# Optimization experiments

Hardware: AMD Instinct MI355X
Metric: run time of the kernel (lower is better)

## Reference

```python
import jax, jax.numpy as jnp
import numpy as np

N = 100_000      # nodes
E = 1_600_000    # edges (avg degree 16)
C_IN, C_H, C_OUT = 32, 64, 64
G = 64           # graphs in batch


def setup_inputs() -> dict:
    key = jax.random.key(0)
    ks = jax.random.split(key, 10)
    x = jax.random.normal(ks[0], (N, C_IN), jnp.float32)
    edge_index = jax.random.randint(ks[1], (2, E), 0, N, dtype=jnp.int64)
    edge_weight = jax.random.uniform(ks[2], (E,), jnp.float32)
    batch = jnp.sort(jax.random.randint(ks[3], (N,), 0, G, dtype=jnp.int64))
    def lin(k, fan_in, fan_out):
        return jax.random.normal(k, (fan_in, fan_out), jnp.float32) / np.float32(np.sqrt(fan_in))
    W1 = lin(ks[4], C_IN, C_H)
    W2 = lin(ks[5], C_H, C_H)
    W3 = lin(ks[6], C_H, C_OUT)
    b1 = jnp.zeros((C_H,), jnp.float32)
    b2 = jnp.zeros((C_H,), jnp.float32)
    b3 = jnp.zeros((C_OUT,), jnp.float32)
    return {"x": x, "edge_weight": edge_weight, "W1": W1, "b1": b1,
            "W2": W2, "b2": b2, "W3": W3, "b3": b3,
            "edge_index": edge_index, "batch": batch}


def _gcn_norm(edge_index, edge_weight, n):
    # PyG GCNConv default: add self-loops (weight 1), symmetric D^-1/2 A D^-1/2 norm.
    loop = jnp.arange(n, dtype=edge_index.dtype)
    src = jnp.concatenate([edge_index[0], loop])
    dst = jnp.concatenate([edge_index[1], loop])
    ew = jnp.concatenate([edge_weight, jnp.ones((n,), edge_weight.dtype)])
    deg = jax.ops.segment_sum(ew, dst, num_segments=n)
    dis = jnp.where(deg > 0, jax.lax.rsqrt(deg), jnp.float32(0))
    norm = dis[src] * ew * dis[dst]
    return src, dst, norm


def _gcn_layer(h, W, b, src, dst, norm, n):
    h = h @ W                                 # [N, out]
    msg = h[src] * norm[:, None]              # gather + scale  [E+N, out]
    agg = jax.ops.segment_sum(msg, dst, num_segments=n)
    return agg + b


def reference(x, edge_weight, W1, b1, W2, b2, W3, b3, edge_index, batch):
    n = x.shape[0]
    src, dst, norm = _gcn_norm(edge_index, edge_weight, n)  # shared across layers
    h = jax.nn.silu(_gcn_layer(x, W1, b1, src, dst, norm, n))
    # Dropout(0.1) is identity in eval mode
    h = jax.nn.silu(_gcn_layer(h, W2, b2, src, dst, norm, n))
    h = jax.nn.silu(_gcn_layer(h, W3, b3, src, dst, norm, n))
    # global_mean_pool over graphs
    sums = jax.ops.segment_sum(h, batch, num_segments=G)
    counts = jax.ops.segment_sum(jnp.ones((n,), h.dtype), batch, num_segments=G)
    return sums / jnp.maximum(counts, 1)[:, None]
```

## Files before the change

kernel.cpp:

```cpp
#include <hip/hip_runtime.h>
#include <hip/hip_fp16.h>
#include <math.h>


#define NB   256
#define PBLK 1024
#define FIXP_SCALE 1048576.0f
#define FIXP_MASK  ((1ULL << 40) - 1)

__device__ __forceinline__ int lower_bound_i(const int* __restrict__ a, int n, int v) {
    int lo = 0, hi = n;
    while (lo < hi) {
        int m = (lo + hi) >> 1;
        if (a[m] < v) lo = m + 1; else hi = m;
    }
    return lo;
}

__global__ __launch_bounds__(256) void k_bhist(const int* __restrict__ dst,
                                               int* __restrict__ hcnt, int e) {
    __shared__ int hist[NB];
    int tid = threadIdx.x, blk = blockIdx.x;
    hist[tid] = 0;
    __syncthreads();
    int chunk = (e + PBLK - 1) / PBLK;
    int lo = blk * chunk, hi = min(e, lo + chunk);
    for (int i = lo + tid; i < hi; i += 256)
        atomicAdd(&hist[dst[i] >> 9], 1);
    __syncthreads();
    hcnt[tid * PBLK + blk] = hist[tid];
}

__global__ __launch_bounds__(256) void k_bscan(int* __restrict__ hcnt,
                                               int* __restrict__ btot) {
    __shared__ int s[256];
    int b = blockIdx.x, tid = threadIdx.x;
    int* row = hcnt + b * PBLK;
    int a0 = row[4 * tid], a1 = row[4 * tid + 1], a2 = row[4 * tid + 2], a3 = row[4 * tid + 3];
    int tsum = a0 + a1 + a2 + a3;
    s[tid] = tsum;
    __syncthreads();
    for (int off = 1; off < 256; off <<= 1) {
        int t = (tid >= off) ? s[tid - off] : 0;
        __syncthreads();
        s[tid] += t;
        __syncthreads();
    }
    int ex = s[tid] - tsum;
    row[4 * tid] = ex;
    row[4 * tid + 1] = ex + a0;
    row[4 * tid + 2] = ex + a0 + a1;
    row[4 * tid + 3] = ex + a0 + a1 + a2;
    if (tid == 255) btot[b] = s[255];
}

__global__ __launch_bounds__(256) void k_bbase(const int* __restrict__ btot,
                                               int* __restrict__ bbase,
                                               int* __restrict__ rowptr, int n, int e) {
    __shared__ int s[256];
    int tid = threadIdx.x;
    int v = btot[tid];
    s[tid] = v;
    __syncthreads();
    for (int off = 1; off < 256; off <<= 1) {
        int t = (tid >= off) ? s[tid - off] : 0;
        __syncthreads();
        s[tid] += t;
        __syncthreads();
    }
    bbase[tid] = s[tid] - v;
    if (tid == 255) bbase[NB] = s[255];
    if (tid == 0) rowptr[n] = e;
}

__global__ __launch_bounds__(256) void k_bpart(const int* __restrict__ src,
                                               const int* __restrict__ dst,
                                               const float* __restrict__ ew,
                                               const int* __restrict__ hcnt,
                                               const int* __restrict__ bbase,
                                               int2* __restrict__ bedge, int e) {
    __shared__ int cur[NB];
    int tid = threadIdx.x, blk = blockIdx.x;
    cur[tid] = bbase[tid] + hcnt[tid * PBLK + blk];
    __syncthreads();
    int chunk = (e + PBLK - 1) / PBLK;
    int lo = blk * chunk, hi = min(e, lo + chunk);
    for (int i = lo + tid; i < hi; i += 256) {
        int d = dst[i];
        int pos = atomicAdd(&cur[d >> 9], 1);
        bedge[pos] = make_int2(src[i] | ((d & 511) << 17), __float_as_int(ew[i]));
    }
}

__global__ __launch_bounds__(256) void k_bucket(const int2* __restrict__ bedge,
                                                const int* __restrict__ bbase,
                                                float* __restrict__ dis,
                                                int* __restrict__ rowptr,
                                                int2* __restrict__ em, int n) {
    __shared__ unsigned long long pk[512];
    __shared__ int cnt[512];
    __shared__ int scn[512];
    __shared__ float sdis[512];
    __shared__ int cur[512];
    int b = blockIdx.x, tid = threadIdx.x;
    int e0 = bbase[b], e1 = bbase[b + 1];
    pk[tid] = 0ULL; pk[tid + 256] = 0ULL;
    __syncthreads();
    for (int i = e0 + tid; i < e1; i += 256) {
        int2 v = bedge[i];
        int dlo = (v.x >> 17) & 511;
        unsigned long long p =
            (1ULL << 40) | (unsigned long long)(__int_as_float(v.y) * FIXP_SCALE);
        atomicAdd(&pk[dlo], p);
    }
    __syncthreads();
#pragma unroll
    for (int k = 0; k < 2; ++k) {
        int i = tid + k * 256;
        unsigned long long v = pk[i];
        int c = (int)(v >> 40);
        cnt[i] = c; scn[i] = c;
        sdis[i] = rsqrtf(1.0f + (float)(v & FIXP_MASK) * (1.0f / FIXP_SCALE));
    }
    __syncthreads();
    for (int off = 1; off < 512; off <<= 1) {
        int i0 = tid, i1 = tid + 256;
        int v0 = (i0 >= off) ? scn[i0 - off] : 0;
        int v1 = (i1 >= off) ? scn[i1 - off] : 0;
        __syncthreads();
        scn[i0] += v0; scn[i1] += v1;
        __syncthreads();
    }
#pragma unroll
    for (int k = 0; k < 2; ++k) {
        int i = tid + k * 256;
        int rb = e0 + scn[i] - cnt[i];
        cur[i] = rb;
        int node = (b << 9) + i;
        if (node < n) { rowptr[node] = rb; dis[node] = sdis[i]; }
    }
    __syncthreads();
    for (int i = e0 + tid; i < e1; i += 256) {
        int2 v = bedge[i];
        int dlo = (v.x >> 17) & 511;
        int pos = atomicAdd(&cur[dlo], 1);
        float w = __int_as_float(v.y) * sdis[dlo];
        em[pos] = make_int2(v.x & 0x1FFFF, __float_as_int(w));
    }
}

__global__ void k_scale(const float* __restrict__ x, const float* __restrict__ dis,
                        __half* __restrict__ hs, int total) {
    int idx = blockIdx.x * blockDim.x + threadIdx.x;
    if (idx < total) hs[idx] = __float2half(x[idx] * dis[idx >> 5]);
}

__device__ __forceinline__ float2 cvt_pair(unsigned int u) {
    __half2 h2 = *(__half2*)&u;
    return __half22float2(h2);
}

template <bool SCALE, typename OUT>
__global__ __launch_bounds__(256, 3) void k_aggmm64(const __half* __restrict__ h,
                                                    const int2* __restrict__ em,
                                                    const int* __restrict__ rowptr,
                                                    const float* __restrict__ dis,
                                                    const float* __restrict__ W,
                                                    const float* __restrict__ bias,
                                                    OUT* __restrict__ out, int n) {
    __shared__ __align__(16) float sacc[4][64];
    __shared__ __align__(8) int2 sme[4][64];
    int lane = threadIdx.x & 63, wv = threadIdx.x >> 6;
    int c = lane & 31, half = lane >> 5;
    const unsigned int* h32 = (const unsigned int*)h;
    float w[64];
#pragma unroll
    for (int k = 0; k < 64; ++k) w[k] = W[k * 64 + lane];
    float bv = bias[lane];
    int wid = (blockIdx.x * blockDim.x + threadIdx.x) >> 6;
    int nw = (gridDim.x * blockDim.x) >> 6;
    for (int node = wid; node < n; node += nw) {
#pragma unroll
        for (int k = 0; k < 64; ++k) asm volatile("" : "+v"(w[k]));
        int lo = rowptr[node], hi = rowptr[node + 1];
        int deg = hi - lo;
        float2 acc = make_float2(0.0f, 0.0f);
        if (half == 0) {
            float2 hv0 = cvt_pair(h32[(unsigned)(node * 32 + c)]);
            float di = dis[node];
            acc.x = di * hv0.x; acc.y = di * hv0.y;
        }
        for (int jb = 0; jb < deg; jb += 64) {
            int idx = lo + jb + lane;
            int2 me = (idx < hi) ? em[idx] : make_int2(0, 0);
            sme[wv][lane] = me;
            int rem = deg - jb;
#pragma unroll
            for (int g = 0; g < 4; ++g) {
                if (g * 16 < rem) {
                    int2 ev[8];
#pragma unroll
                    for (int t = 0; t < 8; ++t)
                        ev[t] = sme[wv][g * 16 + 2 * t + half];
                    unsigned int hv[8];
#pragma unroll
                    for (int t = 0; t < 8; ++t)
                        hv[t] = h32[(unsigned)(ev[t].x * 32 + c)];
#pragma unroll
                    for (int t = 0; t < 8; ++t) {
                        float ww = __int_as_float(ev[t].y);
                        float2 hf = cvt_pair(hv[t]);
                        acc.x = fmaf(ww, hf.x, acc.x);
                        acc.y = fmaf(ww, hf.y, acc.y);
                    }
                }
            }
        }
        acc.x += __shfl_down(acc.x, 32, 64);
        acc.y += __shfl_down(acc.y, 32, 64);
        if (half == 0) ((float2*)sacc[wv])[c] = acc;
        float o = bv;
        const float4* s4 = (const float4*)sacc[wv];
#pragma unroll
        for (int k4 = 0; k4 < 16; ++k4) {
            float4 a4 = s4[k4];
            o = fmaf(a4.x, w[4 * k4 + 0], o);
            o = fmaf(a4.y, w[4 * k4 + 1], o);
            o = fmaf(a4.z, w[4 * k4 + 2], o);
            o = fmaf(a4.w, w[4 * k4 + 3], o);
        }
        o = o / (1.0f + __expf(-o));
        if (SCALE) o *= dis[node];
        if (sizeof(OUT) == 2) {
            ((__half*)out)[(size_t)node * 64 + lane] = __float2half(o);
        } else {
            ((float*)out)[(size_t)node * 64 + lane] = o;
        }
    }
}

__global__ __launch_bounds__(256, 3) void k_aggmm32(const __half* __restrict__ h,
                                                    const int2* __restrict__ em,
                                                    const int* __restrict__ rowptr,
                                                    const float* __restrict__ dis,
                                                    const float* __restrict__ W,
                                                    const float* __restrict__ bias,
                                                    __half* __restrict__ out, int n) {
    __shared__ __align__(16) float sacc[4][32];
    __shared__ __align__(8) int2 sme[4][64];
    int lane = threadIdx.x & 63, wv = threadIdx.x >> 6;
    int c = lane & 15, quarter = lane >> 4;
    const unsigned int* h32 = (const unsigned int*)h;
    float w[32];
#pragma unroll
    for (int k = 0; k < 32; ++k) w[k] = W[k * 64 + lane];
    float bv = bias[lane];
    int wid = (blockIdx.x * blockDim.x + threadIdx.x) >> 6;
    int nw = (gridDim.x * blockDim.x) >> 6;
    for (int node = wid; node < n; node += nw) {
#pragma unroll
        for (int k = 0; k < 32; ++k) asm volatile("" : "+v"(w[k]));
        int lo = rowptr[node], hi = rowptr[node + 1];
        int deg = hi - lo;
        float2 acc = make_float2(0.0f, 0.0f);
        if (quarter == 0) {
            float2 hv0 = cvt_pair(h32[(unsigned)(node * 16 + c)]);
            float di = dis[node];
            acc.x = di * hv0.x; acc.y = di * hv0.y;
        }
        for (int jb = 0; jb < deg; jb += 64) {
            int idx = lo + jb + lane;
            int2 me = (idx < hi) ? em[idx] : make_int2(0, 0);
            sme[wv][lane] = me;
            int rem = deg - jb;
#pragma unroll
            for (int g = 0; g < 4; ++g) {
                if (g * 16 < rem) {
                    int2 ev[4];
#pragma unroll
                    for (int t = 0; t < 4; ++t)
                        ev[t] = sme[wv][g * 16 + 4 * t + quarter];
                    unsigned int hv[4];
#pragma unroll
                    for (int t = 0; t < 4; ++t)
                        hv[t] = h32[(unsigned)(ev[t].x * 16 + c)];
#pragma unroll
                    for (int t = 0; t < 4; ++t) {
                        float ww = __int_as_float(ev[t].y);
                        float2 hf = cvt_pair(hv[t]);
                        acc.x = fmaf(ww, hf.x, acc.x);
                        acc.y = fmaf(ww, hf.y, acc.y);
                    }
                }
            }
        }
        acc.x += __shfl_down(acc.x, 32, 64);
        acc.y += __shfl_down(acc.y, 32, 64);
        acc.x += __shfl_down(acc.x, 16, 64);
        acc.y += __shfl_down(acc.y, 16, 64);
        if (quarter == 0) ((float2*)sacc[wv])[c] = acc;
        float o = bv;
        const float4* s4 = (const float4*)sacc[wv];
#pragma unroll
        for (int k4 = 0; k4 < 8; ++k4) {
            float4 a4 = s4[k4];
            o = fmaf(a4.x, w[4 * k4 + 0], o);
            o = fmaf(a4.y, w[4 * k4 + 1], o);
            o = fmaf(a4.z, w[4 * k4 + 2], o);
            o = fmaf(a4.w, w[4 * k4 + 3], o);
        }
        o = o / (1.0f + __expf(-o));
        o *= dis[node];
        out[(size_t)node * 64 + lane] = __float2half(o);
    }
}

__global__ void k_pool_partial(const float* __restrict__ h, const int* __restrict__ batch,
                               float* __restrict__ acc, int n) {
    int c = threadIdx.x & 63, r = threadIdx.x >> 6;
    int base = blockIdx.x * 128;
    int end = base + 128; if (end > n) end = n;
    float part = 0.0f;
    int cur = -1;
    for (int i = base + r; i < end; i += 4) {
        int g = batch[i];
        if (g != cur) {
            if (cur >= 0) atomicAdd(&acc[cur * 64 + c], part);
            part = 0.0f;
            cur = g;
        }
        part += h[(size_t)i * 64 + c];
    }
    if (cur >= 0) atomicAdd(&acc[cur * 64 + c], part);
}

__global__ void k_pool_final(const float* __restrict__ acc, const int* __restrict__ batch,
                             float* __restrict__ out, int n) {
    int idx = blockIdx.x * blockDim.x + threadIdx.x;
    int g = idx >> 6;
    int lo = lower_bound_i(batch, n, g);
    int hi = lower_bound_i(batch, n, g + 1);
    int cnt = hi - lo;
    out[idx] = acc[idx] / (float)(cnt > 0 ? cnt : 1);
}

extern "C" void kernel_launch(void* const* d_in, const int* in_sizes, int n_in,
                              void* d_out, int out_size, void* d_ws, size_t ws_size,
                              hipStream_t stream) {
    const float* x   = (const float*)d_in[0];
    const float* ew  = (const float*)d_in[1];
    const float* W1  = (const float*)d_in[2];
    const float* b1  = (const float*)d_in[3];
    const float* W2  = (const float*)d_in[4];
    const float* b2  = (const float*)d_in[5];
    const float* W3  = (const float*)d_in[6];
    const float* b3  = (const float*)d_in[7];
    const int*   eidx  = (const int*)d_in[8];
    const int*   batch = (const int*)d_in[9];
    float* out = (float*)d_out;

    const int E = in_sizes[1];
    const int N = in_sizes[9];
    const int G = 64;
    const int* src = eidx;
    const int* dst = eidx + E;

    char* p = (char*)d_ws;
    __half* A     = (__half*)p;                p += (size_t)N * 64 * sizeof(__half);
    __half* B     = (__half*)p;                p += (size_t)N * 64 * sizeof(__half);
    float* C      = (float*)p;                 p += (size_t)N * 64 * sizeof(float);
    float* dis    = (float*)p;                 p += (size_t)N * sizeof(float);
    int*   rowptr = (int*)p;                   p += (size_t)(N + 1) * sizeof(int);
    int*   bbase  = (int*)p;                   p += (size_t)(NB + 1) * sizeof(int);
    float* acc    = (float*)p;                 p += (size_t)G * 64 * sizeof(float);
    p = (char*)(((uintptr_t)p + 7) & ~(uintptr_t)7);
    int2*  em     = (int2*)p;

    int2* bedge = (int2*)A;
    int*  hcnt  = (int*)B;
    int*  btot  = (int*)B + NB * PBLK;

    const int BT = 256;
    const int FUSED_BLOCKS = 3125;

    k_bhist<<<PBLK, 256, 0, stream>>>(dst, hcnt, E);
    k_bscan<<<NB, 256, 0, stream>>>(hcnt, btot);
    k_bbase<<<1, 256, 0, stream>>>(btot, bbase, rowptr, N, E);
    k_bpart<<<PBLK, 256, 0, stream>>>(src, dst, ew, hcnt, bbase, bedge, E);
    k_bucket<<<NB, 256, 0, stream>>>(bedge, bbase, dis, rowptr, em, N);

    k_scale<<<(N * 32 + BT - 1) / BT, BT, 0, stream>>>(x, dis, (__half*)B, N * 32);
    k_aggmm32<<<FUSED_BLOCKS, BT, 0, stream>>>((__half*)B, em, rowptr, dis, W1, b1, A, N);

    k_aggmm64<true, __half><<<FUSED_BLOCKS, BT, 0, stream>>>(A, em, rowptr, dis, W2, b2, B, N);

    k_aggmm64<false, float><<<FUSED_BLOCKS, BT, 0, stream>>>(B, em, rowptr, dis, W3, b3, C, N);

    hipMemsetAsync(acc, 0, (size_t)G * 64 * sizeof(float), stream);
    k_pool_partial<<<(N + 127) / 128, BT, 0, stream>>>(C, batch, acc, N);
    k_pool_final<<<(G * 64) / BT, BT, 0, stream>>>(acc, batch, out, N);
}
```

Measured before the change: 361.8 us.

## Split fused aggregate-then-matmul into separate node matmul and aggregation kernels

For layers 2 and 3, the dense 64x64 transform now runs first as a standalone per-node kernel with W held in shared memory, producing half-precision Z = Y·W. A lighter aggregation kernel then gathers Z over edges and applies bias, SiLU and the optional degree scale. This removes the 64-register weight array and the per-node shared-memory reduction from the gather kernel, so it can run at higher occupancy. The cost is an extra kernel launch per layer and an extra read and write of the node feature matrix. It also changes rounding, because the matmul result is rounded to fp16 before aggregation.

```diff
diff --git a/kernel.cpp b/kernel.cpp
--- a/kernel.cpp
+++ b/kernel.cpp
@@ -160,35 +160,68 @@
     return __half22float2(h2);
 }
 
+__global__ __launch_bounds__(256, 2) void k_mm64(const __half* __restrict__ y,
+                                                 const float* __restrict__ W,
+                                                 __half* __restrict__ z, int n) {
+    __shared__ float sw[64 * 64];
+#pragma unroll
+    for (int i = 0; i < 16; ++i)
+        sw[threadIdx.x + 256 * i] = W[threadIdx.x + 256 * i];
+    __syncthreads();
+    int node = blockIdx.x * 256 + threadIdx.x;
+    if (node >= n) return;
+    uint4 yp[8];
+    const uint4* yrow = (const uint4*)(y + (size_t)node * 64);
+#pragma unroll
+    for (int i = 0; i < 8; ++i) yp[i] = yrow[i];
+    const unsigned int* ypk = (const unsigned int*)yp;
+    float o[64];
+#pragma unroll
+    for (int j = 0; j < 64; ++j) o[j] = 0.0f;
+#pragma unroll
+    for (int k2 = 0; k2 < 32; ++k2) {
+        float2 yk = cvt_pair(ypk[k2]);
+        const float4* r0 = (const float4*)&sw[(2 * k2) * 64];
+        const float4* r1 = (const float4*)&sw[(2 * k2 + 1) * 64];
+#pragma unroll
+        for (int j4 = 0; j4 < 16; ++j4) {
+            float4 w0 = r0[j4];
+            float4 w1 = r1[j4];
+            o[4 * j4 + 0] = fmaf(yk.y, w1.x, fmaf(yk.x, w0.x, o[4 * j4 + 0]));
+            o[4 * j4 + 1] = fmaf(yk.y, w1.y, fmaf(yk.x, w0.y, o[4 * j4 + 1]));
+            o[4 * j4 + 2] = fmaf(yk.y, w1.z, fmaf(yk.x, w0.z, o[4 * j4 + 2]));
+            o[4 * j4 + 3] = fmaf(yk.y, w1.w, fmaf(yk.x, w0.w, o[4 * j4 + 3]));
+        }
+    }
+    __half2* zrow = (__half2*)(z + (size_t)node * 64);
+#pragma unroll
+    for (int j2 = 0; j2 < 32; ++j2)
+        zrow[j2] = __float22half2_rn(make_float2(o[2 * j2], o[2 * j2 + 1]));
+}
+
 template <bool SCALE, typename OUT>
-__global__ __launch_bounds__(256, 3) void k_aggmm64(const __half* __restrict__ h,
-                                                    const int2* __restrict__ em,
-                                                    const int* __restrict__ rowptr,
-                                                    const float* __restrict__ dis,
-                                                    const float* __restrict__ W,
-                                                    const float* __restrict__ bias,
-                                                    OUT* __restrict__ out, int n) {
-    __shared__ __align__(16) float sacc[4][64];
+__global__ __launch_bounds__(256, 4) void k_agg64(const __half* __restrict__ z,
+                                                  const int2* __restrict__ em,
+                                                  const int* __restrict__ rowptr,
+                                                  const float* __restrict__ dis,
+                                                  const float* __restrict__ bias,
+                                                  OUT* __restrict__ out, int n) {
     __shared__ __align__(8) int2 sme[4][64];
     int lane = threadIdx.x & 63, wv = threadIdx.x >> 6;
     int c = lane & 31, half = lane >> 5;
-    const unsigned int* h32 = (const unsigned int*)h;
-    float w[64];
-#pragma unroll
-    for (int k = 0; k < 64; ++k) w[k] = W[k * 64 + lane];
-    float bv = bias[lane];
+    const unsigned int* h32 = (const unsigned int*)z;
+    float2 bv2 = ((const float2*)bias)[c];
     int wid = (blockIdx.x * blockDim.x + threadIdx.x) >> 6;
     int nw = (gridDim.x * blockDim.x) >> 6;
     for (int node = wid; node < n; node += nw) {
-#pragma unroll
-        for (int k = 0; k < 64; ++k) asm volatile("" : "+v"(w[k]));
         int lo = rowptr[node], hi = rowptr[node + 1];
         int deg = hi - lo;
+        float di = 0.0f;
         float2 acc = make_float2(0.0f, 0.0f);
         if (half == 0) {
-            float2 hv0 = cvt_pair(h32[(unsigned)(node * 32 + c)]);
-            float di = dis[node];
-            acc.x = di * hv0.x; acc.y = di * hv0.y;
+            di = dis[node];
+            float2 hv = cvt_pair(h32[(unsigned)(node * 32 + c)]);
+            acc.x = di * hv.x; acc.y = di * hv.y;
         }
         for (int jb = 0; jb < deg; jb += 64) {
             int idx = lo + jb + lane;
@@ -218,23 +251,17 @@
         }
         acc.x += __shfl_down(acc.x, 32, 64);
         acc.y += __shfl_down(acc.y, 32, 64);
-        if (half == 0) ((float2*)sacc[wv])[c] = acc;
-        float o = bv;
-        const float4* s4 = (const float4*)sacc[wv];
-#pragma unroll
-        for (int k4 = 0; k4 < 16; ++k4) {
-            float4 a4 = s4[k4];
-            o = fmaf(a4.x, w[4 * k4 + 0], o);
-            o = fmaf(a4.y, w[4 * k4 + 1], o);
-            o = fmaf(a4.z, w[4 * k4 + 2], o);
-            o = fmaf(a4.w, w[4 * k4 + 3], o);
-        }
-        o = o / (1.0f + __expf(-o));
-        if (SCALE) o *= dis[node];
-        if (sizeof(OUT) == 2) {
-            ((__half*)out)[(size_t)node * 64 + lane] = __float2half(o);
-        } else {
-            ((float*)out)[(size_t)node * 64 + lane] = o;
+        if (half == 0) {
+            float ox = acc.x + bv2.x, oy = acc.y + bv2.y;
+            ox = ox / (1.0f + __expf(-ox));
+            oy = oy / (1.0f + __expf(-oy));
+            if (SCALE) { ox *= di; oy *= di; }
+            if (sizeof(OUT) == 2) {
+                ((__half2*)out)[(size_t)node * 32 + c] =
+                    __float22half2_rn(make_float2(ox, oy));
+            } else {
+                ((float2*)out)[(size_t)node * 32 + c] = make_float2(ox, oy);
+            }
         }
     }
 }
@@ -382,6 +409,7 @@
 
     const int BT = 256;
     const int FUSED_BLOCKS = 3125;
+    const int MM_BLOCKS = (N + 255) / 256;
 
     k_bhist<<<PBLK, 256, 0, stream>>>(dst, hcnt, E);
     k_bscan<<<NB, 256, 0, stream>>>(hcnt, btot);
@@ -392,9 +420,11 @@
     k_scale<<<(N * 32 + BT - 1) / BT, BT, 0, stream>>>(x, dis, (__half*)B, N * 32);
     k_aggmm32<<<FUSED_BLOCKS, BT, 0, stream>>>((__half*)B, em, rowptr, dis, W1, b1, A, N);
 
-    k_aggmm64<true, __half><<<FUSED_BLOCKS, BT, 0, stream>>>(A, em, rowptr, dis, W2, b2, B, N);
-
-    k_aggmm64<false, float><<<FUSED_BLOCKS, BT, 0, stream>>>(B, em, rowptr, dis, W3, b3, C, N);
+    k_mm64<<<MM_BLOCKS, BT, 0, stream>>>(A, W2, B, N);
+    k_agg64<true, __half><<<FUSED_BLOCKS, BT, 0, stream>>>(B, em, rowptr, dis, b2, A, N);
+
+    k_mm64<<<MM_BLOCKS, BT, 0, stream>>>(A, W3, B, N);
+    k_agg64<false, float><<<FUSED_BLOCKS, BT, 0, stream>>>(B, em, rowptr, dis, b3, C, N);
 
     hipMemsetAsync(acc, 0, (size_t)G * 64 * sizeof(float), stream);
     k_pool_partial<<<(N + 127) / 128, BT, 0, stream>>>(C, batch, acc, N);
```

Result: no change. 355.8 us (-1.7%).
